# Performance work log

Measured on AMD Instinct MI355X. Metric: run time of the kernel, lower is better.

## Reference

```python
import jax, jax.numpy as jnp
import numpy as np

D_K = 128

def setup_inputs() -> dict:
    key = jax.random.key(0)
    k1, k2, k3 = jax.random.split(key, 3)
    q = jax.random.normal(k1, (8192, D_K), dtype=jnp.float32)
    k = jax.random.normal(k2, (8192, D_K), dtype=jnp.float32)
    v = jax.random.normal(k3, (8192, D_K), dtype=jnp.float32)
    return {"q": q, "k": k, "v": v}

def reference(q, k, v):
    # scores: [S_q, S_k]
    scores = jnp.einsum('qd,kd->qk', q, k) / jnp.sqrt(jnp.float32(D_K))
    attn = jax.nn.softmax(scores, axis=-1)  # softmax over keys (torch default last dim)
    return jnp.einsum('qk,kd->qd', attn, v)
```

## Files before the change

### kernel.cpp

```cpp
#include <hip/hip_runtime.h>
#include <math.h>


typedef _Float16 f16x8 __attribute__((ext_vector_type(8)));
typedef float    f32x16 __attribute__((ext_vector_type(16)));

constexpr int S_LEN = 8192;
constexpr int D_K   = 128;
constexpr int NSLICE = 8;
constexpr int ITERS2 = (S_LEN / NSLICE) / 64;

constexpr size_t WS_L_OFF = 0;
constexpr size_t KV_OFF   = 262144;
constexpr size_t PART_OFF = KV_OFF + (size_t)256 * 16384;
constexpr size_t WS_NEED  = PART_OFF + (size_t)7 * S_LEN * D_K * 4;

#define CSCALE (0.08838834764831845f * 1.44269504088896340736f)

union UH8 { _Float16 h[8]; uint4 q; f16x8 v; };
union UF4 { unsigned u[4]; uint4 q; f16x8 v; };

__device__ inline void async16(const uint4* g, uint4* l) {
  __builtin_amdgcn_global_load_lds(
      (const __attribute__((address_space(1))) unsigned int*)g,
      (__attribute__((address_space(3))) unsigned int*)l, 16, 0, 0);
}

template <bool ZOUT>
__global__ __launch_bounds__(512) void attn_prep(const float* __restrict__ K,
                                                 const float* __restrict__ V,
                                                 float* __restrict__ out,
                                                 char* __restrict__ ws) {
  const int t = blockIdx.x * 512 + threadIdx.x;
  uint4* KVg = (uint4*)(ws + KV_OFF);
  if (t < 131072) {
    int kt = t >> 9, idx = t & 511;
    int lane = idx & 63, s = idx >> 6;
    int key = kt * 32 + (lane & 31);
    int d0  = s * 16 + (lane >> 5) * 8;
    const float4* src = (const float4*)(K + (size_t)key * D_K + d0);
    float4 a = src[0], b = src[1];
    float f[8] = {a.x, a.y, a.z, a.w, b.x, b.y, b.z, b.w};
    UH8 h;
    #pragma unroll
    for (int j = 0; j < 8; ++j) h.h[j] = (_Float16)f[j];
    KVg[(size_t)kt * 1024 + idx] = h.q;
  } else if (t < 262144) {
    int g = t - 131072;
    int kt = g >> 9, idx = g & 511;
    int lane = idx & 63, c = (idx >> 6) & 3, kstep = idx >> 8;
    int d  = c * 32 + (lane & 31);
    int kb = kt * 32 + kstep * 16 + (lane >> 5) * 8;
    UH8 h;
    #pragma unroll
    for (int j = 0; j < 8; ++j) h.h[j] = (_Float16)V[(size_t)(kb + j) * D_K + d];
    KVg[(size_t)kt * 1024 + 512 + idx] = h.q;
  } else if (ZOUT && t < 327680) {
    int i = t - 262144;
    float4 z = make_float4(0.f, 0.f, 0.f, 0.f);
    float4* o4 = (float4*)out;
    #pragma unroll
    for (int j = 0; j < 4; ++j) o4[(size_t)i * 4 + j] = z;
  } else if (ZOUT && t < 329728) {
    int i = t - 327680;
    ((float4*)(ws + WS_L_OFF))[i] = make_float4(0.f, 0.f, 0.f, 0.f);
  }
}

__device__ inline void qk32(const uint4* sub, const f16x8* qf, int lane,
                            f32x16& Sa, f32x16& Sb) {
  Sa = f32x16{}; Sb = f32x16{};
  __builtin_amdgcn_s_setprio(1);
  #pragma unroll
  for (int s = 0; s < 4; ++s) {
    f16x8 ka = __builtin_bit_cast(f16x8, sub[(2 * s    ) * 64 + lane]);
    f16x8 kb = __builtin_bit_cast(f16x8, sub[(2 * s + 1) * 64 + lane]);
    Sa = __builtin_amdgcn_mfma_f32_32x32x16_f16(ka, qf[2 * s    ], Sa, 0, 0, 0);
    Sb = __builtin_amdgcn_mfma_f32_32x32x16_f16(kb, qf[2 * s + 1], Sb, 0, 0, 0);
  }
  __builtin_amdgcn_s_setprio(0);
}

__device__ inline void softmax32(const f32x16& Sa, const f32x16& Sb,
                                 float& lsum, UF4& A0, UF4& A1) {
  unsigned pk[8];
  #pragma unroll
  for (int i = 0; i < 8; ++i) {
    float p0 = __builtin_amdgcn_exp2f(Sa[2 * i]     + Sb[2 * i]);
    float p1 = __builtin_amdgcn_exp2f(Sa[2 * i + 1] + Sb[2 * i + 1]);
    lsum += p0 + p1;
    pk[i] = __builtin_bit_cast(unsigned, __builtin_amdgcn_cvt_pkrtz(p0, p1));
  }
  auto r0 = __builtin_amdgcn_permlane32_swap((int)pk[0], (int)pk[2], false, false);
  auto r1 = __builtin_amdgcn_permlane32_swap((int)pk[1], (int)pk[3], false, false);
  auto r2 = __builtin_amdgcn_permlane32_swap((int)pk[4], (int)pk[6], false, false);
  auto r3 = __builtin_amdgcn_permlane32_swap((int)pk[5], (int)pk[7], false, false);
  A0.u[0] = (unsigned)r0[0]; A0.u[2] = (unsigned)r0[1];
  A0.u[1] = (unsigned)r1[0]; A0.u[3] = (unsigned)r1[1];
  A1.u[0] = (unsigned)r2[0]; A1.u[2] = (unsigned)r2[1];
  A1.u[1] = (unsigned)r3[0]; A1.u[3] = (unsigned)r3[1];
}

__device__ inline void pv32(const uint4* sub, const UF4& A0, const UF4& A1,
                            int lane, f32x16* O) {
  __builtin_amdgcn_s_setprio(1);
  #pragma unroll
  for (int kstep = 0; kstep < 2; ++kstep) {
    f16x8 pf = kstep ? A1.v : A0.v;
    f16x8 v0 = __builtin_bit_cast(f16x8, sub[512 + kstep * 256 +   0 + lane]);
    f16x8 v1 = __builtin_bit_cast(f16x8, sub[512 + kstep * 256 +  64 + lane]);
    f16x8 v2 = __builtin_bit_cast(f16x8, sub[512 + kstep * 256 + 128 + lane]);
    f16x8 v3 = __builtin_bit_cast(f16x8, sub[512 + kstep * 256 + 192 + lane]);
    O[0] = __builtin_amdgcn_mfma_f32_32x32x16_f16(pf, v0, O[0], 0, 0, 0);
    O[1] = __builtin_amdgcn_mfma_f32_32x32x16_f16(pf, v1, O[1], 0, 0, 0);
    O[2] = __builtin_amdgcn_mfma_f32_32x32x16_f16(pf, v2, O[2], 0, 0, 0);
    O[3] = __builtin_amdgcn_mfma_f32_32x32x16_f16(pf, v3, O[3], 0, 0, 0);
  }
  __builtin_amdgcn_s_setprio(0);
}

template <bool PARTIAL>
__global__ __launch_bounds__(512, 2)
void attn_main(const float* __restrict__ Qg, float* __restrict__ out,
               char* __restrict__ ws) {
  __shared__ uint4 KV[3][2048];

  const int tid   = threadIdx.x;
  const int wave  = tid >> 6;
  const int lane  = tid & 63;
  const int lrow  = lane & 31;
  const int lhalf = lane >> 5;

  const int blk = blockIdx.x;
  const int ks  = blk & 7;
  const int qb  = blk >> 3;
  const int qw  = qb * 256 + wave * 32;

  float* ws_l = (float*)(ws + WS_L_OFF);

  f16x8 qf[8];
  {
    const int q = qw + lrow;
    #pragma unroll
    for (int s = 0; s < 8; ++s) {
      const float4* src = (const float4*)(Qg + (size_t)q * D_K + s * 16 + lhalf * 8);
      float4 a = src[0], b = src[1];
      float f[8] = {a.x, a.y, a.z, a.w, b.x, b.y, b.z, b.w};
      UH8 h;
      #pragma unroll
      for (int j = 0; j < 8; ++j) h.h[j] = (_Float16)(f[j] * CSCALE);
      qf[s] = h.v;
    }
  }

  f32x16 O[4] = {f32x16{}, f32x16{}, f32x16{}, f32x16{}};
  float lsum = 0.f;

  const uint4* KVg = (const uint4*)(ws + KV_OFF);
  const size_t sbase = (size_t)ks * 32768;

  #pragma unroll
  for (int i = 0; i < 4; ++i)
    async16(KVg + sbase + i * 512 + tid, &KV[0][i * 512 + tid]);

  UF4 C00, C01, C10, C11;

  int cur = 0, nxt = 1;
  for (int it = 0; it < ITERS2; ++it) {
    __syncthreads();

    if (it + 1 < ITERS2) {
      const size_t base = sbase + (size_t)(it + 1) * 2048;
      #pragma unroll
      for (int i = 0; i < 4; ++i)
        async16(KVg + base + i * 512 + tid, &KV[nxt][i * 512 + tid]);
    }

    f32x16 Sa0, Sb0, Sa1, Sb1;
    qk32(&KV[cur][0],    qf, lane, Sa0, Sb0);
    qk32(&KV[cur][1024], qf, lane, Sa1, Sb1);

    if (it) {
      const int prv = (cur == 0) ? 2 : cur - 1;
      pv32(&KV[prv][0],    C00, C01, lane, O);
      pv32(&KV[prv][1024], C10, C11, lane, O);
    }

    softmax32(Sa0, Sb0, lsum, C00, C01);
    softmax32(Sa1, Sb1, lsum, C10, C11);

    cur = nxt;
    nxt = (nxt == 2) ? 0 : nxt + 1;
  }
  {
    const int prv = (cur == 0) ? 2 : cur - 1;
    pv32(&KV[prv][0],    C00, C01, lane, O);
    pv32(&KV[prv][1024], C10, C11, lane, O);
  }

  lsum += __shfl_xor(lsum, 32);

  if (PARTIAL) {
    if (lhalf == 0) ws_l[ks * S_LEN + qw + lrow] = lsum;
    float* obase = (ks == 0) ? out
                 : (float*)(ws + PART_OFF) + (size_t)(ks - 1) * S_LEN * D_K;
    #pragma unroll
    for (int r = 0; r < 16; ++r) {
      int row = (r & 3) + 8 * (r >> 2) + 4 * lhalf;
      float* dst = obase + (size_t)(qw + row) * D_K + lrow;
      dst[ 0] = O[0][r];
      dst[32] = O[1][r];
      dst[64] = O[2][r];
      dst[96] = O[3][r];
    }
  } else {
    if (lhalf == 0) atomicAdd(ws_l + qw + lrow, lsum);
    #pragma unroll
    for (int r = 0; r < 16; ++r) {
      int row = (r & 3) + 8 * (r >> 2) + 4 * lhalf;
      float* dst = out + (size_t)(qw + row) * D_K + lrow;
      atomicAdd(dst +  0, O[0][r]);
      atomicAdd(dst + 32, O[1][r]);
      atomicAdd(dst + 64, O[2][r]);
      atomicAdd(dst + 96, O[3][r]);
    }
  }
}

__global__ __launch_bounds__(256) void attn_norm(float* __restrict__ out,
                                                 const float* __restrict__ lpart,
                                                 const float* __restrict__ opart,
                                                 int nparts) {
  int i = blockIdx.x * 256 + threadIdx.x;
  int q = i >> 5;
  float4* o4 = (float4*)out;
  float4 acc = o4[i];
  float l = lpart[q];
  for (int s = 1; s <= nparts; ++s) {
    float4 p = ((const float4*)opart)[(size_t)(s - 1) * 262144 + i];
    acc.x += p.x; acc.y += p.y; acc.z += p.z; acc.w += p.w;
    l += lpart[s * S_LEN + q];
  }
  float inv = 1.0f / l;
  acc.x *= inv; acc.y *= inv; acc.z *= inv; acc.w *= inv;
  o4[i] = acc;
}

extern "C" void kernel_launch(void* const* d_in, const int* in_sizes, int n_in,
                              void* d_out, int out_size, void* d_ws, size_t ws_size,
                              hipStream_t stream) {
  const float* q = (const float*)d_in[0];
  const float* k = (const float*)d_in[1];
  const float* v = (const float*)d_in[2];
  float* out = (float*)d_out;
  char* ws = (char*)d_ws;

  if (ws_size >= WS_NEED) {
    attn_prep<false><<<dim3(512), dim3(512), 0, stream>>>(k, v, out, ws);
    attn_main<true><<<dim3(256), dim3(512), 0, stream>>>(q, out, ws);
    attn_norm<<<dim3(1024), dim3(256), 0, stream>>>(
        out, (const float*)(ws + WS_L_OFF), (const float*)(ws + PART_OFF), 7);
  } else {
    attn_prep<true><<<dim3(645), dim3(512), 0, stream>>>(k, v, out, ws);
    attn_main<false><<<dim3(256), dim3(512), 0, stream>>>(q, out, ws);
    attn_norm<<<dim3(1024), dim3(256), 0, stream>>>(
        out, (const float*)(ws + WS_L_OFF), (const float*)(ws + PART_OFF), 0);
  }
}
```

Before: 109.8 us.

## Split attention waves into QK/softmax producers and PV consumers via LDS

```diff
diff --git a/kernel.cpp b/kernel.cpp
--- a/kernel.cpp
+++ b/kernel.cpp
@@ -67,20 +67,6 @@
   }
 }
 
-__device__ inline void qk32(const uint4* sub, const f16x8* qf, int lane,
-                            f32x16& Sa, f32x16& Sb) {
-  Sa = f32x16{}; Sb = f32x16{};
-  __builtin_amdgcn_s_setprio(1);
-  #pragma unroll
-  for (int s = 0; s < 4; ++s) {
-    f16x8 ka = __builtin_bit_cast(f16x8, sub[(2 * s    ) * 64 + lane]);
-    f16x8 kb = __builtin_bit_cast(f16x8, sub[(2 * s + 1) * 64 + lane]);
-    Sa = __builtin_amdgcn_mfma_f32_32x32x16_f16(ka, qf[2 * s    ], Sa, 0, 0, 0);
-    Sb = __builtin_amdgcn_mfma_f32_32x32x16_f16(kb, qf[2 * s + 1], Sb, 0, 0, 0);
-  }
-  __builtin_amdgcn_s_setprio(0);
-}
-
 __device__ inline void softmax32(const f32x16& Sa, const f32x16& Sb,
                                  float& lsum, UF4& A0, UF4& A1) {
   unsigned pk[8];
@@ -101,45 +87,30 @@
   A1.u[1] = (unsigned)r3[0]; A1.u[3] = (unsigned)r3[1];
 }
 
-__device__ inline void pv32(const uint4* sub, const UF4& A0, const UF4& A1,
-                            int lane, f32x16* O) {
-  __builtin_amdgcn_s_setprio(1);
-  #pragma unroll
-  for (int kstep = 0; kstep < 2; ++kstep) {
-    f16x8 pf = kstep ? A1.v : A0.v;
-    f16x8 v0 = __builtin_bit_cast(f16x8, sub[512 + kstep * 256 +   0 + lane]);
-    f16x8 v1 = __builtin_bit_cast(f16x8, sub[512 + kstep * 256 +  64 + lane]);
-    f16x8 v2 = __builtin_bit_cast(f16x8, sub[512 + kstep * 256 + 128 + lane]);
-    f16x8 v3 = __builtin_bit_cast(f16x8, sub[512 + kstep * 256 + 192 + lane]);
-    O[0] = __builtin_amdgcn_mfma_f32_32x32x16_f16(pf, v0, O[0], 0, 0, 0);
-    O[1] = __builtin_amdgcn_mfma_f32_32x32x16_f16(pf, v1, O[1], 0, 0, 0);
-    O[2] = __builtin_amdgcn_mfma_f32_32x32x16_f16(pf, v2, O[2], 0, 0, 0);
-    O[3] = __builtin_amdgcn_mfma_f32_32x32x16_f16(pf, v3, O[3], 0, 0, 0);
-  }
-  __builtin_amdgcn_s_setprio(0);
-}
-
 template <bool PARTIAL>
 __global__ __launch_bounds__(512, 2)
 void attn_main(const float* __restrict__ Qg, float* __restrict__ out,
                char* __restrict__ ws) {
-  __shared__ uint4 KV[3][2048];
+  __shared__ uint4 Vb[2][1024];
+  __shared__ uint4 Pb[2][1024];
 
   const int tid   = threadIdx.x;
   const int wave  = tid >> 6;
   const int lane  = tid & 63;
   const int lrow  = lane & 31;
   const int lhalf = lane >> 5;
+  const bool isProd = wave < 4;
+  const int  pw   = wave & 3;
 
   const int blk = blockIdx.x;
   const int ks  = blk & 7;
   const int qb  = blk >> 3;
-  const int qw  = qb * 256 + wave * 32;
+  const int qw  = qb * 128 + pw * 32;
 
   float* ws_l = (float*)(ws + WS_L_OFF);
 
   f16x8 qf[8];
-  {
+  if (isProd) {
     const int q = qw + lrow;
     #pragma unroll
     for (int s = 0; s < 8; ++s) {
@@ -159,70 +130,102 @@
   const uint4* KVg = (const uint4*)(ws + KV_OFF);
   const size_t sbase = (size_t)ks * 32768;
 
-  #pragma unroll
-  for (int i = 0; i < 4; ++i)
-    async16(KVg + sbase + i * 512 + tid, &KV[0][i * 512 + tid]);
-
-  UF4 C00, C01, C10, C11;
-
-  int cur = 0, nxt = 1;
-  for (int it = 0; it < ITERS2; ++it) {
+  for (int t = -1; t < ITERS2; ++t) {
+    if (t + 1 < ITERS2) {
+      const size_t nb = sbase + (size_t)(t + 1) * 2048;
+      const int nbuf = (t + 1) & 1;
+      async16(KVg + nb + 512 + tid, &Vb[nbuf][tid]);
+      async16(KVg + nb + 1536 + tid, &Vb[nbuf][512 + tid]);
+
+      if (isProd) {
+        f32x16 Sa0{}, Sb0{}, Sa1{}, Sb1{};
+        __builtin_amdgcn_s_setprio(1);
+        #pragma unroll
+        for (int s = 0; s < 4; ++s) {
+          f16x8 ka = __builtin_bit_cast(f16x8, KVg[nb + (2 * s    ) * 64 + lane]);
+          f16x8 kb = __builtin_bit_cast(f16x8, KVg[nb + (2 * s + 1) * 64 + lane]);
+          Sa0 = __builtin_amdgcn_mfma_f32_32x32x16_f16(ka, qf[2 * s    ], Sa0, 0, 0, 0);
+          Sb0 = __builtin_amdgcn_mfma_f32_32x32x16_f16(kb, qf[2 * s + 1], Sb0, 0, 0, 0);
+        }
+        #pragma unroll
+        for (int s = 0; s < 4; ++s) {
+          f16x8 ka = __builtin_bit_cast(f16x8, KVg[nb + 1024 + (2 * s    ) * 64 + lane]);
+          f16x8 kb = __builtin_bit_cast(f16x8, KVg[nb + 1024 + (2 * s + 1) * 64 + lane]);
+          Sa1 = __builtin_amdgcn_mfma_f32_32x32x16_f16(ka, qf[2 * s    ], Sa1, 0, 0, 0);
+          Sb1 = __builtin_amdgcn_mfma_f32_32x32x16_f16(kb, qf[2 * s + 1], Sb1, 0, 0, 0);
+        }
+        __builtin_amdgcn_s_setprio(0);
+
+        UF4 A00, A01, A10, A11;
+        softmax32(Sa0, Sb0, lsum, A00, A01);
+        softmax32(Sa1, Sb1, lsum, A10, A11);
+        uint4* pd = &Pb[nbuf][pw * 256];
+        pd[lane]       = A00.q;
+        pd[64 + lane]  = A01.q;
+        pd[128 + lane] = A10.q;
+        pd[192 + lane] = A11.q;
+      }
+    }
+
+    if (t >= 0 && !isProd) {
+      const int buf = t & 1;
+      const uint4* pp = &Pb[buf][pw * 256];
+      const uint4* vv = &Vb[buf][0];
+      __builtin_amdgcn_s_setprio(1);
+      #pragma unroll
+      for (int st = 0; st < 2; ++st) {
+        UF4 A0, A1;
+        A0.q = pp[st * 128 + lane];
+        A1.q = pp[st * 128 + 64 + lane];
+        #pragma unroll
+        for (int kstep = 0; kstep < 2; ++kstep) {
+          f16x8 pf = kstep ? A1.v : A0.v;
+          f16x8 v0 = __builtin_bit_cast(f16x8, vv[st * 512 + kstep * 256 +   0 + lane]);
+          f16x8 v1 = __builtin_bit_cast(f16x8, vv[st * 512 + kstep * 256 +  64 + lane]);
+          f16x8 v2 = __builtin_bit_cast(f16x8, vv[st * 512 + kstep * 256 + 128 + lane]);
+          f16x8 v3 = __builtin_bit_cast(f16x8, vv[st * 512 + kstep * 256 + 192 + lane]);
+          O[0] = __builtin_amdgcn_mfma_f32_32x32x16_f16(pf, v0, O[0], 0, 0, 0);
+          O[1] = __builtin_amdgcn_mfma_f32_32x32x16_f16(pf, v1, O[1], 0, 0, 0);
+          O[2] = __builtin_amdgcn_mfma_f32_32x32x16_f16(pf, v2, O[2], 0, 0, 0);
+          O[3] = __builtin_amdgcn_mfma_f32_32x32x16_f16(pf, v3, O[3], 0, 0, 0);
+        }
+      }
+      __builtin_amdgcn_s_setprio(0);
+    }
+
     __syncthreads();
-
-    if (it + 1 < ITERS2) {
-      const size_t base = sbase + (size_t)(it + 1) * 2048;
-      #pragma unroll
-      for (int i = 0; i < 4; ++i)
-        async16(KVg + base + i * 512 + tid, &KV[nxt][i * 512 + tid]);
-    }
-
-    f32x16 Sa0, Sb0, Sa1, Sb1;
-    qk32(&KV[cur][0],    qf, lane, Sa0, Sb0);
-    qk32(&KV[cur][1024], qf, lane, Sa1, Sb1);
-
-    if (it) {
-      const int prv = (cur == 0) ? 2 : cur - 1;
-      pv32(&KV[prv][0],    C00, C01, lane, O);
-      pv32(&KV[prv][1024], C10, C11, lane, O);
-    }
-
-    softmax32(Sa0, Sb0, lsum, C00, C01);
-    softmax32(Sa1, Sb1, lsum, C10, C11);
-
-    cur = nxt;
-    nxt = (nxt == 2) ? 0 : nxt + 1;
-  }
-  {
-    const int prv = (cur == 0) ? 2 : cur - 1;
-    pv32(&KV[prv][0],    C00, C01, lane, O);
-    pv32(&KV[prv][1024], C10, C11, lane, O);
-  }
-
-  lsum += __shfl_xor(lsum, 32);
-
-  if (PARTIAL) {
-    if (lhalf == 0) ws_l[ks * S_LEN + qw + lrow] = lsum;
-    float* obase = (ks == 0) ? out
-                 : (float*)(ws + PART_OFF) + (size_t)(ks - 1) * S_LEN * D_K;
-    #pragma unroll
-    for (int r = 0; r < 16; ++r) {
-      int row = (r & 3) + 8 * (r >> 2) + 4 * lhalf;
-      float* dst = obase + (size_t)(qw + row) * D_K + lrow;
-      dst[ 0] = O[0][r];
-      dst[32] = O[1][r];
-      dst[64] = O[2][r];
-      dst[96] = O[3][r];
+  }
+
+  if (isProd) {
+    lsum += __shfl_xor(lsum, 32);
+    if (PARTIAL) {
+      if (lhalf == 0) ws_l[ks * S_LEN + qw + lrow] = lsum;
+    } else {
+      if (lhalf == 0) atomicAdd(ws_l + qw + lrow, lsum);
     }
   } else {
-    if (lhalf == 0) atomicAdd(ws_l + qw + lrow, lsum);
-    #pragma unroll
-    for (int r = 0; r < 16; ++r) {
-      int row = (r & 3) + 8 * (r >> 2) + 4 * lhalf;
-      float* dst = out + (size_t)(qw + row) * D_K + lrow;
-      atomicAdd(dst +  0, O[0][r]);
-      atomicAdd(dst + 32, O[1][r]);
-      atomicAdd(dst + 64, O[2][r]);
-      atomicAdd(dst + 96, O[3][r]);
+    if (PARTIAL) {
+      float* obase = (ks == 0) ? out
+                   : (float*)(ws + PART_OFF) + (size_t)(ks - 1) * S_LEN * D_K;
+      #pragma unroll
+      for (int r = 0; r < 16; ++r) {
+        int row = (r & 3) + 8 * (r >> 2) + 4 * lhalf;
+        float* dst = obase + (size_t)(qw + row) * D_K + lrow;
+        dst[ 0] = O[0][r];
+        dst[32] = O[1][r];
+        dst[64] = O[2][r];
+        dst[96] = O[3][r];
+      }
+    } else {
+      #pragma unroll
+      for (int r = 0; r < 16; ++r) {
+        int row = (r & 3) + 8 * (r >> 2) + 4 * lhalf;
+        float* dst = out + (size_t)(qw + row) * D_K + lrow;
+        atomicAdd(dst +  0, O[0][r]);
+        atomicAdd(dst + 32, O[1][r]);
+        atomicAdd(dst + 64, O[2][r]);
+        atomicAdd(dst + 96, O[3][r]);
+      }
     }
   }
 }
@@ -257,12 +260,12 @@
 
   if (ws_size >= WS_NEED) {
     attn_prep<false><<<dim3(512), dim3(512), 0, stream>>>(k, v, out, ws);
-    attn_main<true><<<dim3(256), dim3(512), 0, stream>>>(q, out, ws);
+    attn_main<true><<<dim3(512), dim3(512), 0, stream>>>(q, out, ws);
     attn_norm<<<dim3(1024), dim3(256), 0, stream>>>(
         out, (const float*)(ws + WS_L_OFF), (const float*)(ws + PART_OFF), 7);
   } else {
     attn_prep<true><<<dim3(645), dim3(512), 0, stream>>>(k, v, out, ws);
-    attn_main<false><<<dim3(256), dim3(512), 0, stream>>>(q, out, ws);
+    attn_main<false><<<dim3(512), dim3(512), 0, stream>>>(q, out, ws);
     attn_norm<<<dim3(1024), dim3(256), 0, stream>>>(
         out, (const float*)(ws + WS_L_OFF), (const float*)(ws + PART_OFF), 0);
   }
```

Result: slower. 175.1 us (+59.5%).

## Fuse K/V fp16 conversion into main attention kernel, dropping prep pass

Applied to the files above, without the earlier changes.

```diff
diff --git a/kernel.cpp b/kernel.cpp
--- a/kernel.cpp
+++ b/kernel.cpp
@@ -11,8 +11,7 @@
 constexpr int ITERS2 = (S_LEN / NSLICE) / 64;
 
 constexpr size_t WS_L_OFF = 0;
-constexpr size_t KV_OFF   = 262144;
-constexpr size_t PART_OFF = KV_OFF + (size_t)256 * 16384;
+constexpr size_t PART_OFF = 262144;
 constexpr size_t WS_NEED  = PART_OFF + (size_t)7 * S_LEN * D_K * 4;
 
 #define CSCALE (0.08838834764831845f * 1.44269504088896340736f)
@@ -20,65 +19,17 @@
 union UH8 { _Float16 h[8]; uint4 q; f16x8 v; };
 union UF4 { unsigned u[4]; uint4 q; f16x8 v; };
 
-__device__ inline void async16(const uint4* g, uint4* l) {
-  __builtin_amdgcn_global_load_lds(
-      (const __attribute__((address_space(1))) unsigned int*)g,
-      (__attribute__((address_space(3))) unsigned int*)l, 16, 0, 0);
-}
-
-template <bool ZOUT>
-__global__ __launch_bounds__(512) void attn_prep(const float* __restrict__ K,
-                                                 const float* __restrict__ V,
-                                                 float* __restrict__ out,
+__global__ __launch_bounds__(512) void zero_init(float* __restrict__ out,
                                                  char* __restrict__ ws) {
   const int t = blockIdx.x * 512 + threadIdx.x;
-  uint4* KVg = (uint4*)(ws + KV_OFF);
-  if (t < 131072) {
-    int kt = t >> 9, idx = t & 511;
-    int lane = idx & 63, s = idx >> 6;
-    int key = kt * 32 + (lane & 31);
-    int d0  = s * 16 + (lane >> 5) * 8;
-    const float4* src = (const float4*)(K + (size_t)key * D_K + d0);
-    float4 a = src[0], b = src[1];
-    float f[8] = {a.x, a.y, a.z, a.w, b.x, b.y, b.z, b.w};
-    UH8 h;
-    #pragma unroll
-    for (int j = 0; j < 8; ++j) h.h[j] = (_Float16)f[j];
-    KVg[(size_t)kt * 1024 + idx] = h.q;
-  } else if (t < 262144) {
-    int g = t - 131072;
-    int kt = g >> 9, idx = g & 511;
-    int lane = idx & 63, c = (idx >> 6) & 3, kstep = idx >> 8;
-    int d  = c * 32 + (lane & 31);
-    int kb = kt * 32 + kstep * 16 + (lane >> 5) * 8;
-    UH8 h;
-    #pragma unroll
-    for (int j = 0; j < 8; ++j) h.h[j] = (_Float16)V[(size_t)(kb + j) * D_K + d];
-    KVg[(size_t)kt * 1024 + 512 + idx] = h.q;
-  } else if (ZOUT && t < 327680) {
-    int i = t - 262144;
+  if (t < 65536) {
     float4 z = make_float4(0.f, 0.f, 0.f, 0.f);
     float4* o4 = (float4*)out;
     #pragma unroll
-    for (int j = 0; j < 4; ++j) o4[(size_t)i * 4 + j] = z;
-  } else if (ZOUT && t < 329728) {
-    int i = t - 327680;
-    ((float4*)(ws + WS_L_OFF))[i] = make_float4(0.f, 0.f, 0.f, 0.f);
-  }
-}
-
-__device__ inline void qk32(const uint4* sub, const f16x8* qf, int lane,
-                            f32x16& Sa, f32x16& Sb) {
-  Sa = f32x16{}; Sb = f32x16{};
-  __builtin_amdgcn_s_setprio(1);
-  #pragma unroll
-  for (int s = 0; s < 4; ++s) {
-    f16x8 ka = __builtin_bit_cast(f16x8, sub[(2 * s    ) * 64 + lane]);
-    f16x8 kb = __builtin_bit_cast(f16x8, sub[(2 * s + 1) * 64 + lane]);
-    Sa = __builtin_amdgcn_mfma_f32_32x32x16_f16(ka, qf[2 * s    ], Sa, 0, 0, 0);
-    Sb = __builtin_amdgcn_mfma_f32_32x32x16_f16(kb, qf[2 * s + 1], Sb, 0, 0, 0);
-  }
-  __builtin_amdgcn_s_setprio(0);
+    for (int j = 0; j < 4; ++j) o4[(size_t)t * 4 + j] = z;
+  } else if (t < 67584) {
+    ((float4*)(ws + WS_L_OFF))[t - 65536] = make_float4(0.f, 0.f, 0.f, 0.f);
+  }
 }
 
 __device__ inline void softmax32(const f32x16& Sa, const f32x16& Sb,
@@ -99,6 +50,20 @@
   A0.u[1] = (unsigned)r1[0]; A0.u[3] = (unsigned)r1[1];
   A1.u[0] = (unsigned)r2[0]; A1.u[2] = (unsigned)r2[1];
   A1.u[1] = (unsigned)r3[0]; A1.u[3] = (unsigned)r3[1];
+}
+
+__device__ inline void qk32(const uint4* sub, const f16x8* qf, int lane,
+                            f32x16& Sa, f32x16& Sb) {
+  Sa = f32x16{}; Sb = f32x16{};
+  __builtin_amdgcn_s_setprio(1);
+  #pragma unroll
+  for (int s = 0; s < 4; ++s) {
+    f16x8 ka = __builtin_bit_cast(f16x8, sub[(2 * s    ) * 64 + lane]);
+    f16x8 kb = __builtin_bit_cast(f16x8, sub[(2 * s + 1) * 64 + lane]);
+    Sa = __builtin_amdgcn_mfma_f32_32x32x16_f16(ka, qf[2 * s    ], Sa, 0, 0, 0);
+    Sb = __builtin_amdgcn_mfma_f32_32x32x16_f16(kb, qf[2 * s + 1], Sb, 0, 0, 0);
+  }
+  __builtin_amdgcn_s_setprio(0);
 }
 
 __device__ inline void pv32(const uint4* sub, const UF4& A0, const UF4& A1,
@@ -119,9 +84,17 @@
   __builtin_amdgcn_s_setprio(0);
 }
 
+__device__ inline uint4 pack8(const float* f) {
+  UH8 h;
+  #pragma unroll
+  for (int j = 0; j < 8; ++j) h.h[j] = (_Float16)f[j];
+  return h.q;
+}
+
 template <bool PARTIAL>
 __global__ __launch_bounds__(512, 2)
-void attn_main(const float* __restrict__ Qg, float* __restrict__ out,
+void attn_main(const float* __restrict__ Qg, const float* __restrict__ Kg,
+               const float* __restrict__ Vg, float* __restrict__ out,
                char* __restrict__ ws) {
   __shared__ uint4 KV[3][2048];
 
@@ -136,6 +109,12 @@
   const int qb  = blk >> 3;
   const int qw  = qb * 256 + wave * 32;
 
+  const int keybase = ks * (S_LEN / NSLICE);
+
+  const int kd0 = wave * 16 + lhalf * 8;
+  const int vd  = (wave & 3) * 32 + lrow;
+  const int vkb = (wave >> 2) * 16 + lhalf * 8;
+
   float* ws_l = (float*)(ws + WS_L_OFF);
 
   f16x8 qf[8];
@@ -156,12 +135,21 @@
   f32x16 O[4] = {f32x16{}, f32x16{}, f32x16{}, f32x16{}};
   float lsum = 0.f;
 
-  const uint4* KVg = (const uint4*)(ws + KV_OFF);
-  const size_t sbase = (size_t)ks * 32768;
-
-  #pragma unroll
-  for (int i = 0; i < 4; ++i)
-    async16(KVg + sbase + i * 512 + tid, &KV[0][i * 512 + tid]);
+  {
+    const int tb = keybase;
+    #pragma unroll
+    for (int st = 0; st < 2; ++st) {
+      const float* kp = Kg + (size_t)(tb + st * 32 + lrow) * D_K + kd0;
+      float4 a = ((const float4*)kp)[0], b = ((const float4*)kp)[1];
+      float kf[8] = {a.x, a.y, a.z, a.w, b.x, b.y, b.z, b.w};
+      KV[0][st * 1024 + tid] = pack8(kf);
+      const int kb = tb + st * 32 + vkb;
+      float vf[8];
+      #pragma unroll
+      for (int j = 0; j < 8; ++j) vf[j] = Vg[(size_t)(kb + j) * D_K + vd];
+      KV[0][st * 1024 + 512 + tid] = pack8(vf);
+    }
+  }
 
   UF4 C00, C01, C10, C11;
 
@@ -169,21 +157,47 @@
   for (int it = 0; it < ITERS2; ++it) {
     __syncthreads();
 
-    if (it + 1 < ITERS2) {
-      const size_t base = sbase + (size_t)(it + 1) * 2048;
-      #pragma unroll
-      for (int i = 0; i < 4; ++i)
-        async16(KVg + base + i * 512 + tid, &KV[nxt][i * 512 + tid]);
+    const bool doStage = (it + 1 < ITERS2);
+    const int tb = keybase + (it + 1) * 64;
+
+    float4 ka0, kb0, ka1, kb1;
+    if (doStage) {
+      const float* kp0 = Kg + (size_t)(tb +  0 + lrow) * D_K + kd0;
+      const float* kp1 = Kg + (size_t)(tb + 32 + lrow) * D_K + kd0;
+      ka0 = ((const float4*)kp0)[0]; kb0 = ((const float4*)kp0)[1];
+      ka1 = ((const float4*)kp1)[0]; kb1 = ((const float4*)kp1)[1];
     }
 
     f32x16 Sa0, Sb0, Sa1, Sb1;
     qk32(&KV[cur][0],    qf, lane, Sa0, Sb0);
     qk32(&KV[cur][1024], qf, lane, Sa1, Sb1);
+
+    if (doStage) {
+      float k0[8] = {ka0.x, ka0.y, ka0.z, ka0.w, kb0.x, kb0.y, kb0.z, kb0.w};
+      float k1[8] = {ka1.x, ka1.y, ka1.z, ka1.w, kb1.x, kb1.y, kb1.z, kb1.w};
+      KV[nxt][tid]        = pack8(k0);
+      KV[nxt][1024 + tid] = pack8(k1);
+    }
+
+    float v0[8], v1[8];
+    if (doStage) {
+      const int kb0i = tb +  0 + vkb;
+      const int kb1i = tb + 32 + vkb;
+      #pragma unroll
+      for (int j = 0; j < 8; ++j) v0[j] = Vg[(size_t)(kb0i + j) * D_K + vd];
+      #pragma unroll
+      for (int j = 0; j < 8; ++j) v1[j] = Vg[(size_t)(kb1i + j) * D_K + vd];
+    }
 
     if (it) {
       const int prv = (cur == 0) ? 2 : cur - 1;
       pv32(&KV[prv][0],    C00, C01, lane, O);
       pv32(&KV[prv][1024], C10, C11, lane, O);
+    }
+
+    if (doStage) {
+      KV[nxt][512 + tid]  = pack8(v0);
+      KV[nxt][1536 + tid] = pack8(v1);
     }
 
     softmax32(Sa0, Sb0, lsum, C00, C01);
@@ -256,13 +270,12 @@
   char* ws = (char*)d_ws;
 
   if (ws_size >= WS_NEED) {
-    attn_prep<false><<<dim3(512), dim3(512), 0, stream>>>(k, v, out, ws);
-    attn_main<true><<<dim3(256), dim3(512), 0, stream>>>(q, out, ws);
+    attn_main<true><<<dim3(256), dim3(512), 0, stream>>>(q, k, v, out, ws);
     attn_norm<<<dim3(1024), dim3(256), 0, stream>>>(
         out, (const float*)(ws + WS_L_OFF), (const float*)(ws + PART_OFF), 7);
   } else {
-    attn_prep<true><<<dim3(645), dim3(512), 0, stream>>>(k, v, out, ws);
-    attn_main<false><<<dim3(256), dim3(512), 0, stream>>>(q, out, ws);
+    zero_init<<<dim3(132), dim3(512), 0, stream>>>(out, ws);
+    attn_main<false><<<dim3(256), dim3(512), 0, stream>>>(q, k, v, out, ws);
     attn_norm<<<dim3(1024), dim3(256), 0, stream>>>(
         out, (const float*)(ws + WS_L_OFF), (const float*)(ws + PART_OFF), 0);
   }
```

Result: slower. 118.6 us (+8.1%).

## Fuse split-K reduction into main kernel via grid-wide atomic barrier

Applied to the files above, without the earlier changes.

```diff
diff --git a/kernel.cpp b/kernel.cpp
--- a/kernel.cpp
+++ b/kernel.cpp
@@ -13,7 +13,8 @@
 constexpr size_t WS_L_OFF = 0;
 constexpr size_t KV_OFF   = 262144;
 constexpr size_t PART_OFF = KV_OFF + (size_t)256 * 16384;
-constexpr size_t WS_NEED  = PART_OFF + (size_t)7 * S_LEN * D_K * 4;
+constexpr size_t CNT_OFF  = PART_OFF + (size_t)7 * S_LEN * D_K * 4;
+constexpr size_t WS_NEED  = CNT_OFF + 64;
 
 #define CSCALE (0.08838834764831845f * 1.44269504088896340736f)
 
@@ -33,6 +34,7 @@
                                                  char* __restrict__ ws) {
   const int t = blockIdx.x * 512 + threadIdx.x;
   uint4* KVg = (uint4*)(ws + KV_OFF);
+  if (t == 0) *(unsigned*)(ws + CNT_OFF) = 0u;
   if (t < 131072) {
     int kt = t >> 9, idx = t & 511;
     int lane = idx & 63, s = idx >> 6;
@@ -213,6 +215,38 @@
       dst[64] = O[2][r];
       dst[96] = O[3][r];
     }
+
+    unsigned* cnt = (unsigned*)(ws + CNT_OFF);
+    __threadfence();
+    __syncthreads();
+    if (tid == 0) {
+      __hip_atomic_fetch_add(cnt, 1u, __ATOMIC_RELEASE, __HIP_MEMORY_SCOPE_AGENT);
+      while (__hip_atomic_load(cnt, __ATOMIC_ACQUIRE, __HIP_MEMORY_SCOPE_AGENT) < 256u)
+        __builtin_amdgcn_s_sleep(8);
+    }
+    __syncthreads();
+
+    {
+      const float* lpart = ws_l;
+      const float* opart = (const float*)(ws + PART_OFF);
+      float4* o4 = (float4*)out;
+      #pragma unroll
+      for (int j = 0; j < 2; ++j) {
+        const int i = blk * 1024 + j * 512 + tid;
+        const int q = i >> 5;
+        float4 acc = o4[i];
+        float l = lpart[q];
+        #pragma unroll
+        for (int s = 1; s <= 7; ++s) {
+          float4 p = ((const float4*)opart)[(size_t)(s - 1) * 262144 + i];
+          acc.x += p.x; acc.y += p.y; acc.z += p.z; acc.w += p.w;
+          l += lpart[s * S_LEN + q];
+        }
+        float inv = 1.0f / l;
+        acc.x *= inv; acc.y *= inv; acc.z *= inv; acc.w *= inv;
+        o4[i] = acc;
+      }
+    }
   } else {
     if (lhalf == 0) atomicAdd(ws_l + qw + lrow, lsum);
     #pragma unroll
@@ -258,12 +292,10 @@
   if (ws_size >= WS_NEED) {
     attn_prep<false><<<dim3(512), dim3(512), 0, stream>>>(k, v, out, ws);
     attn_main<true><<<dim3(256), dim3(512), 0, stream>>>(q, out, ws);
-    attn_norm<<<dim3(1024), dim3(256), 0, stream>>>(
-        out, (const float*)(ws + WS_L_OFF), (const float*)(ws + PART_OFF), 7);
   } else {
     attn_prep<true><<<dim3(645), dim3(512), 0, stream>>>(k, v, out, ws);
     attn_main<false><<<dim3(256), dim3(512), 0, stream>>>(q, out, ws);
     attn_norm<<<dim3(1024), dim3(256), 0, stream>>>(
-        out, (const float*)(ws + WS_L_OFF), (const float*)(ws + PART_OFF), 0);
-  }
-}
+        out, (const float*)(ws + WS_L_OFF), (const float*)(ws + KV_OFF), 0);
+  }
+}
```

After: 195.0 us. +77.7%, slower.
